# Optimization experiments

Measured on AMD Instinct MI355X. Metric: run time of the kernel, lower is better.

## Reference

```python
import jax, jax.numpy as jnp
import numpy as np

N_NODES = 100000
N_EDGES = 1600000
N_GRAPHS = 1024


def gcn_conv(x, src, dst, W, b, num_nodes):
    # GCNConv: x' = D^{-1/2} (A + I) D^{-1/2} x W + b  (self-loops already appended to src/dst)
    h = x @ W  # [N, out]
    deg = jax.ops.segment_sum(jnp.ones_like(dst, dtype=h.dtype), dst, num_segments=num_nodes)
    dinv = jnp.where(deg > 0, jax.lax.rsqrt(jnp.maximum(deg, 1.0)), 0.0)
    norm = dinv[src] * dinv[dst]  # [E]
    msg = h[src] * norm[:, None]  # [E, out]  <- dominant memory traffic
    return jax.ops.segment_sum(msg, dst, num_segments=num_nodes) + b


def global_mean_pool(x, batch, num_graphs):
    s = jax.ops.segment_sum(x, batch, num_segments=num_graphs)
    cnt = jax.ops.segment_sum(jnp.ones((x.shape[0],), x.dtype), batch, num_segments=num_graphs)
    return s / jnp.maximum(cnt, 1.0)[:, None]


def setup_inputs() -> dict:
    key = jax.random.key(0)
    ks = jax.random.split(key, 12)
    x = jax.random.normal(ks[0], (N_NODES, 4), dtype=jnp.float32)
    edge_index = jax.random.randint(ks[1], (2, N_EDGES), 0, N_NODES, dtype=jnp.int64)
    batch = jnp.sort(jax.random.randint(ks[2], (N_NODES,), 0, N_GRAPHS, dtype=jnp.int64))
    def glorot(k, shape):
        fan = shape[0] + shape[1]
        return jax.random.normal(k, shape, jnp.float32) * jnp.sqrt(2.0 / fan)
    return {
        "x": x, "edge_index": edge_index, "batch": batch,
        "W1": glorot(ks[3], (4, 64)),   "b1": jnp.zeros((64,), jnp.float32),
        "W2": glorot(ks[4], (64, 128)), "b2": jnp.zeros((128,), jnp.float32),
        "fc1_W": glorot(ks[5], (128, 64)), "fc1_b": jnp.zeros((64,), jnp.float32),
        "fc2_W": glorot(ks[6], (64, 1)),   "fc2_b": jnp.zeros((1,), jnp.float32),
    }


def reference(x, edge_index, batch, W1, b1, W2, b2, fc1_W, fc1_b, fc2_W, fc2_b):
    n = x.shape[0]
    loops = jnp.arange(n, dtype=edge_index.dtype)
    src = jnp.concatenate([edge_index[0], loops])
    dst = jnp.concatenate([edge_index[1], loops])
    h = jax.nn.relu(gcn_conv(x, src, dst, W1, b1, n))
    h = jax.nn.relu(gcn_conv(h, src, dst, W2, b2, n))
    g = global_mean_pool(h, batch, N_GRAPHS)  # [G, 128]
    g = jax.nn.relu(g @ fc1_W + fc1_b)
    return g @ fc2_W + fc2_b  # [G, 1]
```

## Files before the change

### kernel.cpp

```cpp
#include <hip/hip_runtime.h>
#include <math.h>


#define EPB 8192
#define BSH 8
#define NBUK_MAX 512

__global__ void k_bukhist(const int* __restrict__ dst, int E,
                          int* __restrict__ bkcnt, int nbuk) {
  __shared__ int hist[NBUK_MAX];
  for (int i = threadIdx.x; i < nbuk; i += blockDim.x) hist[i] = 0;
  __syncthreads();
  int i0 = blockIdx.x * EPB, i1 = min(i0 + EPB, E);
  for (int i = i0 + threadIdx.x; i < i1; i += blockDim.x)
    atomicAdd(&hist[dst[i] >> BSH], 1);
  __syncthreads();
  for (int i = threadIdx.x; i < nbuk; i += blockDim.x)
    if (hist[i]) atomicAdd(&bkcnt[i], hist[i]);
}

__global__ void k_scan_buk(const int* __restrict__ bkcnt, int* __restrict__ bcur,
                           int nbuk) {
  __shared__ int sh[NBUK_MAX];
  int t = threadIdx.x;
  int v = (t < nbuk) ? bkcnt[t] : 0;
  sh[t] = v;
  __syncthreads();
  for (int o = 1; o < NBUK_MAX; o <<= 1) {
    int u = (t >= o) ? sh[t - o] : 0;
    __syncthreads();
    sh[t] += u;
    __syncthreads();
  }
  if (t < nbuk) bcur[t] = sh[t] - v;
}

__global__ void k_bucket(const int* __restrict__ src, const int* __restrict__ dst,
                         int E, int* __restrict__ bcur, int* __restrict__ ebuf,
                         int nbuk) {
  __shared__ int hist[NBUK_MAX];
  __shared__ int hbase[NBUK_MAX];
  int t = threadIdx.x;
  int i0 = blockIdx.x * EPB, i1 = min(i0 + EPB, E);
  for (int i = t; i < nbuk; i += blockDim.x) hist[i] = 0;
  __syncthreads();
  for (int i = i0 + t; i < i1; i += blockDim.x)
    atomicAdd(&hist[dst[i] >> BSH], 1);
  __syncthreads();
  for (int i = t; i < nbuk; i += blockDim.x) {
    int c = hist[i];
    hbase[i] = c ? atomicAdd(&bcur[i], c) : 0;
  }
  __syncthreads();
  for (int i = t; i < nbuk; i += blockDim.x) hist[i] = 0;
  __syncthreads();
  for (int i = i0 + t; i < i1; i += blockDim.x) {
    int d = dst[i];
    int b = d >> BSH;
    int pos = hbase[b] + atomicAdd(&hist[b], 1);
    ebuf[pos] = src[i] | ((d & 255) << 17);
  }
}

__global__ void __launch_bounds__(256) k_sortfill(
    const int* __restrict__ ebuf, const int* __restrict__ bcur,
    int* __restrict__ row_ptr, int* __restrict__ csr_src, int N, int nbuk) {
  __shared__ int hist[256];
  __shared__ int sc[256];
  __shared__ int cur[256];
  int b = blockIdx.x, t = threadIdx.x;
  int e0 = (b == 0) ? 0 : bcur[b - 1];
  int e1 = bcur[b];
  hist[t] = 0;
  __syncthreads();
  for (int i = e0 + t; i < e1; i += 256)
    atomicAdd(&hist[ebuf[i] >> 17], 1);
  __syncthreads();
  int v = hist[t];
  sc[t] = v;
  __syncthreads();
  for (int o = 1; o < 256; o <<= 1) {
    int u = (t >= o) ? sc[t - o] : 0;
    __syncthreads();
    sc[t] += u;
    __syncthreads();
  }
  int excl = sc[t] - v;
  int node = (b << BSH) + t;
  if (node < N) row_ptr[node] = e0 + excl;
  if (b == nbuk - 1 && t == 0) row_ptr[N] = e1;
  cur[t] = excl;
  __syncthreads();
  for (int i = e0 + t; i < e1; i += 256) {
    int e = ebuf[i];
    int pos = e0 + atomicAdd(&cur[e >> 17], 1);
    csr_src[pos] = e & 0x1FFFF;
  }
}

__global__ void k_prep(const int* __restrict__ row_ptr, const float* __restrict__ x,
                       float* __restrict__ dinv, float* __restrict__ xp, int N) {
  int i = blockIdx.x * blockDim.x + threadIdx.x;
  if (i < N) {
    int deg = row_ptr[i + 1] - row_ptr[i];
    float di = 1.0f / sqrtf((float)(deg + 1));
    dinv[i] = di;
    float4 v = ((const float4*)x)[i];
    v.x *= di; v.y *= di; v.z *= di; v.w *= di;
    ((float4*)xp)[i] = v;
  }
}

__global__ void k_conv1(const float* __restrict__ xp, const int* __restrict__ row_ptr,
                        const int* __restrict__ csr_src, const float* __restrict__ dinv,
                        const float* __restrict__ W1, const float* __restrict__ b1,
                        float* __restrict__ h1p, int N) {
  int lane = threadIdx.x & 63;
  int sub = lane >> 4, sl = lane & 15;
  int wid = (blockIdx.x * blockDim.x + threadIdx.x) >> 6;
  int nw = (gridDim.x * blockDim.x) >> 6;
  const float4* x4 = (const float4*)xp;
  float w1 = W1[lane], w2 = W1[64 + lane], w3 = W1[128 + lane], w4 = W1[192 + lane];
  float bb = b1[lane];
  for (int base = wid * 4; base < N; base += nw * 4) {
    int n = base + sub;
    bool valid = (n < N);
    int e0 = 0, e1 = 0;
    if (valid) { e0 = row_ptr[n]; e1 = row_ptr[n + 1]; }
    float ax = 0.f, ay = 0.f, az = 0.f, aw = 0.f;
    for (int j = e0 + sl; j < e1; j += 16) {
      float4 xs = x4[csr_src[j]];
      ax += xs.x; ay += xs.y; az += xs.z; aw += xs.w;
    }
#pragma unroll
    for (int o = 8; o; o >>= 1) {
      ax += __shfl_xor(ax, o); ay += __shfl_xor(ay, o);
      az += __shfl_xor(az, o); aw += __shfl_xor(aw, o);
    }
    float di = 0.f;
    if (valid) {
      di = dinv[n];
      float4 xn = x4[n];
      ax += xn.x; ay += xn.y; az += xn.z; aw += xn.w;
    }
#pragma unroll
    for (int g = 0; g < 4; ++g) {
      int nn = base + g;
      if (nn < N) {
        int srcl = g * 16;
        float bx = __shfl(ax, srcl), by = __shfl(ay, srcl);
        float bz = __shfl(az, srcl), bw = __shfl(aw, srcl);
        float dg = __shfl(di, srcl);
        float o0 = bb;
        o0 = fmaf(bx * dg, w1, o0);
        o0 = fmaf(by * dg, w2, o0);
        o0 = fmaf(bz * dg, w3, o0);
        o0 = fmaf(bw * dg, w4, o0);
        h1p[(size_t)nn * 64 + lane] = fmaxf(o0, 0.f) * dg;
      }
    }
  }
}

__global__ void __launch_bounds__(256) k_agg2(
    const float* __restrict__ h1p, const int* __restrict__ row_ptr,
    const int* __restrict__ csr_src, const float* __restrict__ dinv,
    float* __restrict__ agg, int N) {
  int lane = threadIdx.x & 63;
  int wid = (blockIdx.x * blockDim.x + threadIdx.x) >> 6;
  int nw = (gridDim.x * blockDim.x) >> 6;
  for (int n = wid; n < N; n += nw) {
    int e0 = row_ptr[n], e1 = row_ptr[n + 1];
    float a0 = 0.f, a1 = 0.f, a2 = 0.f, a3 = 0.f;
    float a4 = 0.f, a5 = 0.f, a6 = 0.f, a7 = 0.f;
    int j = e0;
    for (; j + 8 <= e1; j += 8) {
      int s0 = csr_src[j + 0], s1 = csr_src[j + 1];
      int s2 = csr_src[j + 2], s3 = csr_src[j + 3];
      int s4 = csr_src[j + 4], s5 = csr_src[j + 5];
      int s6 = csr_src[j + 6], s7 = csr_src[j + 7];
      a0 += h1p[(size_t)s0 * 64 + lane]; a1 += h1p[(size_t)s1 * 64 + lane];
      a2 += h1p[(size_t)s2 * 64 + lane]; a3 += h1p[(size_t)s3 * 64 + lane];
      a4 += h1p[(size_t)s4 * 64 + lane]; a5 += h1p[(size_t)s5 * 64 + lane];
      a6 += h1p[(size_t)s6 * 64 + lane]; a7 += h1p[(size_t)s7 * 64 + lane];
    }
    for (; j + 2 <= e1; j += 2) {
      int s0 = csr_src[j], s1 = csr_src[j + 1];
      a0 += h1p[(size_t)s0 * 64 + lane]; a1 += h1p[(size_t)s1 * 64 + lane];
    }
    if (j < e1) a0 += h1p[(size_t)csr_src[j] * 64 + lane];
    float acc = ((a0 + a1) + (a2 + a3)) + ((a4 + a5) + (a6 + a7));
    acc += h1p[(size_t)n * 64 + lane];
    agg[(size_t)n * 64 + lane] = acc * dinv[n];
  }
}

__global__ void __launch_bounds__(256, 4) k_mm2pool(
    const float* __restrict__ agg, const int* __restrict__ batch,
    const float* __restrict__ W2, const float* __restrict__ b2,
    float* __restrict__ gsum, int N) {
  __shared__ float aT[64][36];
  __shared__ int gid_s[32];
  int tid = threadIdx.x;
  int base = blockIdx.x * 32;
  const float4* agg4 = (const float4*)agg;
  for (int idx = tid; idx < 32 * 16; idx += 256) {
    int node = idx >> 4, chunk = idx & 15;
    int n = base + node;
    float4 v = make_float4(0.f, 0.f, 0.f, 0.f);
    if (n < N) v = agg4[(size_t)n * 16 + chunk];
    aT[chunk * 4 + 0][node] = v.x;
    aT[chunk * 4 + 1][node] = v.y;
    aT[chunk * 4 + 2][node] = v.z;
    aT[chunk * 4 + 3][node] = v.w;
  }
  if (tid < 32) {
    int n = base + tid;
    gid_s[tid] = (n < N) ? batch[n] : -1;
  }
  __syncthreads();
  int c = tid & 127;
  int g = tid >> 7;
  float acc[16];
#pragma unroll
  for (int i = 0; i < 16; ++i) acc[i] = 0.f;
#pragma unroll 4
  for (int k = 0; k < 64; ++k) {
    float w = W2[k * 128 + c];
    const float4* ap = (const float4*)&aT[k][g * 16];
    float4 v0 = ap[0], v1 = ap[1], v2 = ap[2], v3 = ap[3];
    acc[0] = fmaf(v0.x, w, acc[0]);  acc[1] = fmaf(v0.y, w, acc[1]);
    acc[2] = fmaf(v0.z, w, acc[2]);  acc[3] = fmaf(v0.w, w, acc[3]);
    acc[4] = fmaf(v1.x, w, acc[4]);  acc[5] = fmaf(v1.y, w, acc[5]);
    acc[6] = fmaf(v1.z, w, acc[6]);  acc[7] = fmaf(v1.w, w, acc[7]);
    acc[8] = fmaf(v2.x, w, acc[8]);  acc[9] = fmaf(v2.y, w, acc[9]);
    acc[10] = fmaf(v2.z, w, acc[10]); acc[11] = fmaf(v2.w, w, acc[11]);
    acc[12] = fmaf(v3.x, w, acc[12]); acc[13] = fmaf(v3.y, w, acc[13]);
    acc[14] = fmaf(v3.z, w, acc[14]); acc[15] = fmaf(v3.w, w, acc[15]);
  }
  float bias = b2[c];
  float run = 0.f;
  int cur = -1;
#pragma unroll
  for (int i = 0; i < 16; ++i) {
    int n = base + g * 16 + i;
    if (n < N) {
      int gg = gid_s[g * 16 + i];
      float v = fmaxf(acc[i] + bias, 0.f);
      if (gg == cur) {
        run += v;
      } else {
        if (cur >= 0) atomicAdd(&gsum[(size_t)cur * 128 + c], run);
        cur = gg;
        run = v;
      }
    }
  }
  if (cur >= 0) atomicAdd(&gsum[(size_t)cur * 128 + c], run);
}

__device__ __forceinline__ int lower_bound(const int* __restrict__ a, int n, int key) {
  int lo = 0, hi = n;
  while (lo < hi) {
    int m = (lo + hi) >> 1;
    if (a[m] < key) lo = m + 1; else hi = m;
  }
  return lo;
}

__global__ void k_fc(const float* __restrict__ gsum, const int* __restrict__ batch,
                     const float* __restrict__ fc1W, const float* __restrict__ fc1b,
                     const float* __restrict__ fc2W, const float* __restrict__ fc2b,
                     float* __restrict__ out, int N, int G) {
  int g = blockIdx.x;
  int tid = threadIdx.x;
  __shared__ int bnd[2];
  if (tid == 0) bnd[0] = lower_bound(batch, N, g);
  if (tid == 1) bnd[1] = lower_bound(batch, N, g + 1);
  __shared__ float grow[128];
  __syncthreads();
  int cnt = bnd[1] - bnd[0];
  float inv = 1.0f / (float)max(cnt, 1);
  grow[tid] = gsum[(size_t)g * 128 + tid] * inv;
  __syncthreads();
  if (tid < 64) {
    float o = fc1b[tid];
#pragma unroll 8
    for (int k = 0; k < 128; ++k) o = fmaf(grow[k], fc1W[k * 64 + tid], o);
    o = fmaxf(o, 0.f);
    float v = o * fc2W[tid];
#pragma unroll
    for (int off = 32; off; off >>= 1) v += __shfl_xor(v, off);
    if (tid == 0) out[g] = v + fc2b[0];
  }
}

extern "C" void kernel_launch(void* const* d_in, const int* in_sizes, int n_in,
                              void* d_out, int out_size, void* d_ws, size_t ws_size,
                              hipStream_t stream) {
  const float* x = (const float*)d_in[0];
  const int* ei = (const int*)d_in[1];
  const int* batch = (const int*)d_in[2];
  const float* W1 = (const float*)d_in[3];
  const float* b1 = (const float*)d_in[4];
  const float* W2 = (const float*)d_in[5];
  const float* b2 = (const float*)d_in[6];
  const float* fc1W = (const float*)d_in[7];
  const float* fc1b = (const float*)d_in[8];
  const float* fc2W = (const float*)d_in[9];
  const float* fc2b = (const float*)d_in[10];
  float* out = (float*)d_out;

  int N = in_sizes[0] / 4;
  int E = in_sizes[1] / 2;
  int G = out_size;
  const int* src = ei;
  const int* dst = ei + E;

  char* ws = (char*)d_ws;
  size_t off = 0;
  auto take = [&](size_t b) {
    char* p = ws + off;
    off += (b + 255) & ~(size_t)255;
    return p;
  };
  int nbuk = (N + 255) >> BSH;
  int ebl = (E + EPB - 1) / EPB;
  int* row_ptr  = (int*)take((size_t)(N + 1) * 4);
  int* bkcnt    = (int*)take((size_t)NBUK_MAX * 4);
  int* bcur     = (int*)take((size_t)NBUK_MAX * 4);
  float* dinv   = (float*)take((size_t)N * 4);
  float* xp     = (float*)take((size_t)N * 4 * 4);
  int* ebuf     = (int*)take((size_t)E * 4);
  int* csr_src  = (int*)take((size_t)E * 4);
  float* h1p    = (float*)take((size_t)N * 64 * 4);
  float* agg    = (float*)take((size_t)N * 64 * 4);
  float* gsum   = (float*)take((size_t)G * 128 * 4);
  (void)ws_size;

  hipMemsetAsync(bkcnt, 0, (size_t)NBUK_MAX * 4, stream);
  hipMemsetAsync(gsum, 0, (size_t)G * 128 * 4, stream);

  k_bukhist<<<ebl, 256, 0, stream>>>(dst, E, bkcnt, nbuk);
  k_scan_buk<<<1, NBUK_MAX, 0, stream>>>(bkcnt, bcur, nbuk);
  k_bucket<<<ebl, 256, 0, stream>>>(src, dst, E, bcur, ebuf, nbuk);
  k_sortfill<<<nbuk, 256, 0, stream>>>(ebuf, bcur, row_ptr, csr_src, N, nbuk);

  k_prep<<<(N + 255) / 256, 256, 0, stream>>>(row_ptr, x, dinv, xp, N);
  k_conv1<<<2048, 256, 0, stream>>>(xp, row_ptr, csr_src, dinv, W1, b1, h1p, N);
  k_agg2<<<4096, 256, 0, stream>>>(h1p, row_ptr, csr_src, dinv, agg, N);
  k_mm2pool<<<(N + 31) / 32, 256, 0, stream>>>(agg, batch, W2, b2, gsum, N);
  k_fc<<<G, 128, 0, stream>>>(gsum, batch, fc1W, fc1b, fc2W, fc2b, out, N, G);
}
```

Baseline: 271.2 us.

## Fuse aggregation with W2 matmul, sort CSR rows, and pool deterministically

Several changes at once. The degree-normalisation prep is folded into the CSR sort-fill kernel, and each row's source indices are sorted (insertion sort in LDS when the bucket fits) to improve gather locality. The layer-2 aggregation is fused with the W2 matmul, writing full h2 rows; mean pooling moves into the FC kernel via segment scans instead of atomics. EPB is also reduced. The cost is an extra N×128 h2 write and read in exchange for dropping the agg buffer round trip and the atomics.

```diff
diff --git a/kernel.cpp b/kernel.cpp
--- a/kernel.cpp
+++ b/kernel.cpp
@@ -2,9 +2,10 @@
 #include <math.h>
 
 
-#define EPB 8192
+#define EPB 2048
 #define BSH 8
 #define NBUK_MAX 512
+#define SFCAP 5120
 
 __global__ void k_bukhist(const int* __restrict__ dst, int E,
                           int* __restrict__ bkcnt, int nbuk) {
@@ -64,13 +65,18 @@
 
 __global__ void __launch_bounds__(256) k_sortfill(
     const int* __restrict__ ebuf, const int* __restrict__ bcur,
-    int* __restrict__ row_ptr, int* __restrict__ csr_src, int N, int nbuk) {
+    const float* __restrict__ x, int* __restrict__ row_ptr,
+    int* __restrict__ csr_src, float* __restrict__ dinv,
+    float* __restrict__ xp, int N, int nbuk) {
   __shared__ int hist[256];
   __shared__ int sc[256];
   __shared__ int cur[256];
+  __shared__ int buf[SFCAP];
   int b = blockIdx.x, t = threadIdx.x;
   int e0 = (b == 0) ? 0 : bcur[b - 1];
   int e1 = bcur[b];
+  int cnt = e1 - e0;
+  bool inlds = (cnt <= SFCAP);
   hist[t] = 0;
   __syncthreads();
   for (int i = e0 + t; i < e1; i += 256)
@@ -87,28 +93,45 @@
   }
   int excl = sc[t] - v;
   int node = (b << BSH) + t;
-  if (node < N) row_ptr[node] = e0 + excl;
+  if (node < N) {
+    row_ptr[node] = e0 + excl;
+    float di = 1.0f / sqrtf((float)(v + 1));
+    dinv[node] = di;
+    float4 xv = ((const float4*)x)[node];
+    xv.x *= di; xv.y *= di; xv.z *= di; xv.w *= di;
+    ((float4*)xp)[node] = xv;
+  }
   if (b == nbuk - 1 && t == 0) row_ptr[N] = e1;
   cur[t] = excl;
   __syncthreads();
   for (int i = e0 + t; i < e1; i += 256) {
     int e = ebuf[i];
-    int pos = e0 + atomicAdd(&cur[e >> 17], 1);
-    csr_src[pos] = e & 0x1FFFF;
-  }
-}
-
-__global__ void k_prep(const int* __restrict__ row_ptr, const float* __restrict__ x,
-                       float* __restrict__ dinv, float* __restrict__ xp, int N) {
-  int i = blockIdx.x * blockDim.x + threadIdx.x;
-  if (i < N) {
-    int deg = row_ptr[i + 1] - row_ptr[i];
-    float di = 1.0f / sqrtf((float)(deg + 1));
-    dinv[i] = di;
-    float4 v = ((const float4*)x)[i];
-    v.x *= di; v.y *= di; v.z *= di; v.w *= di;
-    ((float4*)xp)[i] = v;
-  }
+    int pos = atomicAdd(&cur[e >> 17], 1);
+    if (inlds) buf[pos] = e & 0x1FFFF;
+    else csr_src[e0 + pos] = e & 0x1FFFF;
+  }
+  __syncthreads();
+  if (node < N && v > 1) {
+    if (inlds) {
+      for (int i = 1; i < v; ++i) {
+        int key = buf[excl + i];
+        int j = i - 1;
+        while (j >= 0 && buf[excl + j] > key) { buf[excl + j + 1] = buf[excl + j]; --j; }
+        buf[excl + j + 1] = key;
+      }
+    } else {
+      int s0 = e0 + excl;
+      for (int i = 1; i < v; ++i) {
+        int key = csr_src[s0 + i];
+        int j = i - 1;
+        while (j >= 0 && csr_src[s0 + j] > key) { csr_src[s0 + j + 1] = csr_src[s0 + j]; --j; }
+        csr_src[s0 + j + 1] = key;
+      }
+    }
+  }
+  __syncthreads();
+  if (inlds)
+    for (int i = t; i < cnt; i += 256) csr_src[e0 + i] = buf[i];
 }
 
 __global__ void k_conv1(const float* __restrict__ xp, const int* __restrict__ row_ptr,
@@ -162,101 +185,67 @@
   }
 }
 
-__global__ void __launch_bounds__(256) k_agg2(
+__global__ void __launch_bounds__(256) k_aggmm(
     const float* __restrict__ h1p, const int* __restrict__ row_ptr,
     const int* __restrict__ csr_src, const float* __restrict__ dinv,
-    float* __restrict__ agg, int N) {
-  int lane = threadIdx.x & 63;
-  int wid = (blockIdx.x * blockDim.x + threadIdx.x) >> 6;
-  int nw = (gridDim.x * blockDim.x) >> 6;
-  for (int n = wid; n < N; n += nw) {
-    int e0 = row_ptr[n], e1 = row_ptr[n + 1];
-    float a0 = 0.f, a1 = 0.f, a2 = 0.f, a3 = 0.f;
-    float a4 = 0.f, a5 = 0.f, a6 = 0.f, a7 = 0.f;
-    int j = e0;
-    for (; j + 8 <= e1; j += 8) {
-      int s0 = csr_src[j + 0], s1 = csr_src[j + 1];
-      int s2 = csr_src[j + 2], s3 = csr_src[j + 3];
-      int s4 = csr_src[j + 4], s5 = csr_src[j + 5];
-      int s6 = csr_src[j + 6], s7 = csr_src[j + 7];
-      a0 += h1p[(size_t)s0 * 64 + lane]; a1 += h1p[(size_t)s1 * 64 + lane];
-      a2 += h1p[(size_t)s2 * 64 + lane]; a3 += h1p[(size_t)s3 * 64 + lane];
-      a4 += h1p[(size_t)s4 * 64 + lane]; a5 += h1p[(size_t)s5 * 64 + lane];
-      a6 += h1p[(size_t)s6 * 64 + lane]; a7 += h1p[(size_t)s7 * 64 + lane];
-    }
-    for (; j + 2 <= e1; j += 2) {
-      int s0 = csr_src[j], s1 = csr_src[j + 1];
-      a0 += h1p[(size_t)s0 * 64 + lane]; a1 += h1p[(size_t)s1 * 64 + lane];
-    }
-    if (j < e1) a0 += h1p[(size_t)csr_src[j] * 64 + lane];
-    float acc = ((a0 + a1) + (a2 + a3)) + ((a4 + a5) + (a6 + a7));
-    acc += h1p[(size_t)n * 64 + lane];
-    agg[(size_t)n * 64 + lane] = acc * dinv[n];
-  }
-}
-
-__global__ void __launch_bounds__(256, 4) k_mm2pool(
-    const float* __restrict__ agg, const int* __restrict__ batch,
     const float* __restrict__ W2, const float* __restrict__ b2,
-    float* __restrict__ gsum, int N) {
-  __shared__ float aT[64][36];
-  __shared__ int gid_s[32];
+    float* __restrict__ h2, int N) {
+  __shared__ float aT[64][20];
   int tid = threadIdx.x;
-  int base = blockIdx.x * 32;
-  const float4* agg4 = (const float4*)agg;
-  for (int idx = tid; idx < 32 * 16; idx += 256) {
-    int node = idx >> 4, chunk = idx & 15;
-    int n = base + node;
-    float4 v = make_float4(0.f, 0.f, 0.f, 0.f);
-    if (n < N) v = agg4[(size_t)n * 16 + chunk];
-    aT[chunk * 4 + 0][node] = v.x;
-    aT[chunk * 4 + 1][node] = v.y;
-    aT[chunk * 4 + 2][node] = v.z;
-    aT[chunk * 4 + 3][node] = v.w;
-  }
-  if (tid < 32) {
-    int n = base + tid;
-    gid_s[tid] = (n < N) ? batch[n] : -1;
+  int lane = tid & 63;
+  int w = tid >> 6;
+  int base = blockIdx.x * 16;
+  for (int ln = 0; ln < 4; ++ln) {
+    int n = base + w * 4 + ln;
+    float acc = 0.f;
+    if (n < N) {
+      int e0 = row_ptr[n], e1 = row_ptr[n + 1];
+      float a0 = 0.f, a1 = 0.f, a2 = 0.f, a3 = 0.f;
+      float a4 = 0.f, a5 = 0.f, a6 = 0.f, a7 = 0.f;
+      int j = e0;
+      for (; j + 8 <= e1; j += 8) {
+        int s0 = csr_src[j + 0], s1 = csr_src[j + 1];
+        int s2 = csr_src[j + 2], s3 = csr_src[j + 3];
+        int s4 = csr_src[j + 4], s5 = csr_src[j + 5];
+        int s6 = csr_src[j + 6], s7 = csr_src[j + 7];
+        a0 += h1p[(size_t)s0 * 64 + lane]; a1 += h1p[(size_t)s1 * 64 + lane];
+        a2 += h1p[(size_t)s2 * 64 + lane]; a3 += h1p[(size_t)s3 * 64 + lane];
+        a4 += h1p[(size_t)s4 * 64 + lane]; a5 += h1p[(size_t)s5 * 64 + lane];
+        a6 += h1p[(size_t)s6 * 64 + lane]; a7 += h1p[(size_t)s7 * 64 + lane];
+      }
+      for (; j + 2 <= e1; j += 2) {
+        int s0 = csr_src[j], s1 = csr_src[j + 1];
+        a0 += h1p[(size_t)s0 * 64 + lane]; a1 += h1p[(size_t)s1 * 64 + lane];
+      }
+      if (j < e1) a0 += h1p[(size_t)csr_src[j] * 64 + lane];
+      acc = ((a0 + a1) + (a2 + a3)) + ((a4 + a5) + (a6 + a7));
+      acc += h1p[(size_t)n * 64 + lane];
+      acc *= dinv[n];
+    }
+    aT[lane][w * 4 + ln] = acc;
   }
   __syncthreads();
   int c = tid & 127;
   int g = tid >> 7;
-  float acc[16];
-#pragma unroll
-  for (int i = 0; i < 16; ++i) acc[i] = 0.f;
+  float acc[8];
+#pragma unroll
+  for (int i = 0; i < 8; ++i) acc[i] = 0.f;
 #pragma unroll 4
   for (int k = 0; k < 64; ++k) {
-    float w = W2[k * 128 + c];
-    const float4* ap = (const float4*)&aT[k][g * 16];
-    float4 v0 = ap[0], v1 = ap[1], v2 = ap[2], v3 = ap[3];
-    acc[0] = fmaf(v0.x, w, acc[0]);  acc[1] = fmaf(v0.y, w, acc[1]);
-    acc[2] = fmaf(v0.z, w, acc[2]);  acc[3] = fmaf(v0.w, w, acc[3]);
-    acc[4] = fmaf(v1.x, w, acc[4]);  acc[5] = fmaf(v1.y, w, acc[5]);
-    acc[6] = fmaf(v1.z, w, acc[6]);  acc[7] = fmaf(v1.w, w, acc[7]);
-    acc[8] = fmaf(v2.x, w, acc[8]);  acc[9] = fmaf(v2.y, w, acc[9]);
-    acc[10] = fmaf(v2.z, w, acc[10]); acc[11] = fmaf(v2.w, w, acc[11]);
-    acc[12] = fmaf(v3.x, w, acc[12]); acc[13] = fmaf(v3.y, w, acc[13]);
-    acc[14] = fmaf(v3.z, w, acc[14]); acc[15] = fmaf(v3.w, w, acc[15]);
+    float wv = W2[k * 128 + c];
+    const float4* ap = (const float4*)&aT[k][g * 8];
+    float4 v0 = ap[0], v1 = ap[1];
+    acc[0] = fmaf(v0.x, wv, acc[0]); acc[1] = fmaf(v0.y, wv, acc[1]);
+    acc[2] = fmaf(v0.z, wv, acc[2]); acc[3] = fmaf(v0.w, wv, acc[3]);
+    acc[4] = fmaf(v1.x, wv, acc[4]); acc[5] = fmaf(v1.y, wv, acc[5]);
+    acc[6] = fmaf(v1.z, wv, acc[6]); acc[7] = fmaf(v1.w, wv, acc[7]);
   }
   float bias = b2[c];
-  float run = 0.f;
-  int cur = -1;
-#pragma unroll
-  for (int i = 0; i < 16; ++i) {
-    int n = base + g * 16 + i;
-    if (n < N) {
-      int gg = gid_s[g * 16 + i];
-      float v = fmaxf(acc[i] + bias, 0.f);
-      if (gg == cur) {
-        run += v;
-      } else {
-        if (cur >= 0) atomicAdd(&gsum[(size_t)cur * 128 + c], run);
-        cur = gg;
-        run = v;
-      }
-    }
-  }
-  if (cur >= 0) atomicAdd(&gsum[(size_t)cur * 128 + c], run);
+#pragma unroll
+  for (int i = 0; i < 8; ++i) {
+    int n = base + g * 8 + i;
+    if (n < N) h2[(size_t)n * 128 + c] = fmaxf(acc[i] + bias, 0.f);
+  }
 }
 
 __device__ __forceinline__ int lower_bound(const int* __restrict__ a, int n, int key) {
@@ -268,30 +257,40 @@
   return lo;
 }
 
-__global__ void k_fc(const float* __restrict__ gsum, const int* __restrict__ batch,
-                     const float* __restrict__ fc1W, const float* __restrict__ fc1b,
-                     const float* __restrict__ fc2W, const float* __restrict__ fc2b,
-                     float* __restrict__ out, int N, int G) {
+__global__ void k_pool_fc(const float* __restrict__ h2, const int* __restrict__ batch,
+                          const float* __restrict__ fc1W, const float* __restrict__ fc1b,
+                          const float* __restrict__ fc2W, const float* __restrict__ fc2b,
+                          float* __restrict__ out, int N, int G) {
   int g = blockIdx.x;
-  int tid = threadIdx.x;
-  __shared__ int bnd[2];
-  if (tid == 0) bnd[0] = lower_bound(batch, N, g);
-  if (tid == 1) bnd[1] = lower_bound(batch, N, g + 1);
+  __shared__ int bounds[2];
+  if (threadIdx.x == 0) bounds[0] = lower_bound(batch, N, g);
+  if (threadIdx.x == 1) bounds[1] = lower_bound(batch, N, g + 1);
+  __syncthreads();
+  int beg = bounds[0], end = bounds[1];
+  int c = threadIdx.x & 127;
+  int gr = threadIdx.x >> 7;
+  float acc = 0.f;
+  for (int i = beg + gr; i < end; i += 2) acc += h2[(size_t)i * 128 + c];
+  __shared__ float red[256];
   __shared__ float grow[128];
-  __syncthreads();
-  int cnt = bnd[1] - bnd[0];
-  float inv = 1.0f / (float)max(cnt, 1);
-  grow[tid] = gsum[(size_t)g * 128 + tid] * inv;
-  __syncthreads();
-  if (tid < 64) {
-    float o = fc1b[tid];
+  red[threadIdx.x] = acc;
+  __syncthreads();
+  if (threadIdx.x < 128) {
+    float s = red[threadIdx.x] + red[threadIdx.x + 128];
+    int cnt = end - beg;
+    grow[threadIdx.x] = s / (float)max(cnt, 1);
+  }
+  __syncthreads();
+  if (threadIdx.x < 64) {
+    int c1 = threadIdx.x;
+    float o = fc1b[c1];
 #pragma unroll 8
-    for (int k = 0; k < 128; ++k) o = fmaf(grow[k], fc1W[k * 64 + tid], o);
+    for (int k = 0; k < 128; ++k) o = fmaf(grow[k], fc1W[k * 64 + c1], o);
     o = fmaxf(o, 0.f);
-    float v = o * fc2W[tid];
+    float v = o * fc2W[c1];
 #pragma unroll
     for (int off = 32; off; off >>= 1) v += __shfl_xor(v, off);
-    if (tid == 0) out[g] = v + fc2b[0];
+    if (c1 == 0) out[g] = v + fc2b[0];
   }
 }
 
@@ -334,21 +333,17 @@
   int* ebuf     = (int*)take((size_t)E * 4);
   int* csr_src  = (int*)take((size_t)E * 4);
   float* h1p    = (float*)take((size_t)N * 64 * 4);
-  float* agg    = (float*)take((size_t)N * 64 * 4);
-  float* gsum   = (float*)take((size_t)G * 128 * 4);
+  float* h2     = (float*)take((size_t)N * 128 * 4);
   (void)ws_size;
 
   hipMemsetAsync(bkcnt, 0, (size_t)NBUK_MAX * 4, stream);
-  hipMemsetAsync(gsum, 0, (size_t)G * 128 * 4, stream);
 
   k_bukhist<<<ebl, 256, 0, stream>>>(dst, E, bkcnt, nbuk);
   k_scan_buk<<<1, NBUK_MAX, 0, stream>>>(bkcnt, bcur, nbuk);
   k_bucket<<<ebl, 256, 0, stream>>>(src, dst, E, bcur, ebuf, nbuk);
-  k_sortfill<<<nbuk, 256, 0, stream>>>(ebuf, bcur, row_ptr, csr_src, N, nbuk);
-
-  k_prep<<<(N + 255) / 256, 256, 0, stream>>>(row_ptr, x, dinv, xp, N);
+  k_sortfill<<<nbuk, 256, 0, stream>>>(ebuf, bcur, x, row_ptr, csr_src, dinv, xp, N, nbuk);
+
   k_conv1<<<2048, 256, 0, stream>>>(xp, row_ptr, csr_src, dinv, W1, b1, h1p, N);
-  k_agg2<<<4096, 256, 0, stream>>>(h1p, row_ptr, csr_src, dinv, agg, N);
-  k_mm2pool<<<(N + 31) / 32, 256, 0, stream>>>(agg, batch, W2, b2, gsum, N);
-  k_fc<<<G, 128, 0, stream>>>(gsum, batch, fc1W, fc1b, fc2W, fc2b, out, N, G);
-}
+  k_aggmm<<<(N + 15) / 16, 256, 0, stream>>>(h1p, row_ptr, csr_src, dinv, W2, b2, h2, N);
+  k_pool_fc<<<G, 256, 0, stream>>>(h2, batch, fc1W, fc1b, fc2W, fc2b, out, N, G);
+}
```

Result: slower. 320.8 us (+18.3%).
